# Performance work log

Measured on AMD Instinct MI355X. Metric: run time of the kernel, lower is better.

The kernel has to match this reference:

```python
import jax, jax.numpy as jnp
import numpy as np

NUM_CLASSES = 100


def setup_inputs() -> dict:
    key = jax.random.key(0)
    k1, k2, k3, k4 = jax.random.split(key, 4)
    x = jax.random.normal(k1, (256, 2048), dtype=jnp.float32)
    W_model = jax.random.normal(k2, (2048, 64), dtype=jnp.float32)
    database_code = jax.random.normal(k3, (100000, 64), dtype=jnp.float32)
    database_labels = jax.random.randint(k4, (100000,), 0, NUM_CLASSES, dtype=jnp.int64)
    return {
        "x": x,
        "W_model": W_model,
        "database_code": database_code,
        "database_labels": database_labels,
        "K": 1000,
    }


def reference(x, W_model, database_code, database_labels, K):
    # model(x): single linear projection to hash-code space [B, d]
    out = x @ W_model
    # sim_score = out @ codes.T * -0.5 + num_classes/2  -> [B, N]
    sim = jnp.matmul(out, database_code.T) * -0.5 + NUM_CLASSES / 2
    # np.argpartition(sim, K)[:, :K] selects the K SMALLEST scores.
    # Equivalent set via top_k on negated scores.
    _, topk_idx = jax.lax.top_k(-sim, K)            # [B, K]
    topk_labels = database_labels[topk_idx]          # [B, K]
    # per-class histogram over the top-K retrieved labels
    classes = jnp.arange(NUM_CLASSES, dtype=topk_labels.dtype)
    counts = (topk_labels[:, :, None] == classes[None, None, :]).sum(axis=1)  # [B, C]
    probs = counts.astype(jnp.float32) / K
    return probs
```

## Files before the change

kernel.cpp:

```cpp
#include <hip/hip_runtime.h>
#include <hip/hip_fp16.h>


#define NBK 256
#define FNB 1024
#define CAPC 2048
#define BCAP 2048
#define MROWS 32
#define NCHX 64
#define NCLS 100

typedef _Float16 half8 __attribute__((ext_vector_type(8)));
typedef float floatx4 __attribute__((ext_vector_type(4)));

static __device__ __forceinline__ unsigned packh2(float a, float b) {
  _Float16 ha = (_Float16)a, hb = (_Float16)b;
  unsigned short ua, ub;
  __builtin_memcpy(&ua, &ha, 2); __builtin_memcpy(&ub, &hb, 2);
  return (unsigned)ua | ((unsigned)ub << 16);
}

static __device__ __forceinline__ void rowRange(double b1sq, double cmax,
                                                double& lo, double& inv, double& bw) {
  double hr = 0.5 * sqrt(b1sq * cmax) * 1.000001 + 9.0;
  lo = 50.0 - hr;
  bw = (2.0 * hr) / (double)NBK;
  inv = (double)NBK / (2.0 * hr);
}

static __device__ __forceinline__ void loadA(const unsigned short* __restrict__ out16,
                                             int m0, int mr, int quad,
                                             half8& a00, half8& a01, half8& a10, half8& a11) {
  const uint4* o4 = (const uint4*)out16;
  uint4 u;
  u = o4[(size_t)(m0 + mr) * 8 + quad];          __builtin_memcpy(&a00, &u, 16);
  u = o4[(size_t)(m0 + mr) * 8 + 4 + quad];      __builtin_memcpy(&a01, &u, 16);
  u = o4[(size_t)(m0 + 16 + mr) * 8 + quad];     __builtin_memcpy(&a10, &u, 16);
  u = o4[(size_t)(m0 + 16 + mr) * 8 + 4 + quad]; __builtin_memcpy(&a11, &u, 16);
}

__global__ __launch_bounds__(1024) void k_prep(const float* __restrict__ x,
                                               const float* __restrict__ W,
                                               const float* __restrict__ codes,
                                               const int* __restrict__ labels,
                                               int N, int Npad, int D, int B, int nCvt,
                                               unsigned short* __restrict__ codes16,
                                               float* __restrict__ cmaxSlab,
                                               double* __restrict__ out64,
                                               unsigned short* __restrict__ out16,
                                               double* __restrict__ B1sq,
                                               int* __restrict__ shiftp) {
  __shared__ double red[1024];
  __shared__ float xs[2048];
  __shared__ float fredw[16];
  __shared__ int flag;
  int blk = (int)blockIdx.x, tid = (int)threadIdx.x;
  int lane = tid & 63, wid = tid >> 6;
  if (blk < nCvt) {
    int gl = tid & 15, g = tid >> 4;
    int base = blk * 256;
    int r0 = base + g, r1 = base + 64 + g, r2 = base + 128 + g, r3 = base + 192 + g;
    float4 q0 = {0.f,0.f,0.f,0.f}, q1 = q0, q2 = q0, q3 = q0;
    if (r0 < N) q0 = ((const float4*)(codes + (size_t)r0 * 64))[gl];
    if (r1 < N) q1 = ((const float4*)(codes + (size_t)r1 * 64))[gl];
    if (r2 < N) q2 = ((const float4*)(codes + (size_t)r2 * 64))[gl];
    if (r3 < N) q3 = ((const float4*)(codes + (size_t)r3 * 64))[gl];
    uint2 o0, o1, o2, o3;
    o0.x = packh2(q0.x, q0.y); o0.y = packh2(q0.z, q0.w);
    o1.x = packh2(q1.x, q1.y); o1.y = packh2(q1.z, q1.w);
    o2.x = packh2(q2.x, q2.y); o2.y = packh2(q2.z, q2.w);
    o3.x = packh2(q3.x, q3.y); o3.y = packh2(q3.z, q3.w);
    ((uint2*)(codes16 + (size_t)r0 * 64))[gl] = o0;
    ((uint2*)(codes16 + (size_t)r1 * 64))[gl] = o1;
    ((uint2*)(codes16 + (size_t)r2 * 64))[gl] = o2;
    ((uint2*)(codes16 + (size_t)r3 * 64))[gl] = o3;
    float bmax = 0.0f;
#define NRM(qv)                                                            \
    { double c2 = fma((double)(qv).x, (double)(qv).x, 0.0);                \
      c2 = fma((double)(qv).y, (double)(qv).y, c2);                        \
      c2 = fma((double)(qv).z, (double)(qv).z, c2);                        \
      c2 = fma((double)(qv).w, (double)(qv).w, c2);                        \
      c2 += __shfl_xor(c2, 1, 16); c2 += __shfl_xor(c2, 2, 16);            \
      c2 += __shfl_xor(c2, 4, 16); c2 += __shfl_xor(c2, 8, 16);            \
      bmax = fmaxf(bmax, (float)(c2 * 1.000001)); }
    NRM(q0) NRM(q1) NRM(q2) NRM(q3)
#undef NRM
#pragma unroll
    for (int off = 32; off > 0; off >>= 1) bmax = fmaxf(bmax, __shfl_xor(bmax, off, 64));
    if (lane == 0) fredw[wid] = bmax;
    __syncthreads();
    if (tid == 0) {
      float m = fredw[0];
#pragma unroll
      for (int j = 1; j < 16; ++j) m = fmaxf(m, fredw[j]);
      cmaxSlab[blk] = m;
    }
  } else if (blk < nCvt + B) {
    int b = blk - nCvt;
    const float* xr = x + (size_t)b * D;
    for (int i = tid; i < (D >> 1); i += 1024)
      ((float2*)xs)[i] = ((const float2*)xr)[i];
    __syncthreads();
    int t = tid & 63, w = tid >> 6;
    int kc = D >> 4;
    int k0 = w * kc;
    double a[8];
#pragma unroll
    for (int j = 0; j < 8; ++j) a[j] = 0.0;
#pragma unroll 2
    for (int k = k0; k < k0 + kc; k += 8) {
#pragma unroll
      for (int j = 0; j < 8; ++j)
        a[j] = fma((double)xs[k + j], (double)W[(size_t)(k + j) * 64 + t], a[j]);
    }
    red[tid] = ((a[0] + a[1]) + (a[2] + a[3])) + ((a[4] + a[5]) + (a[6] + a[7]));
    __syncthreads();
    if (w == 0) {
      double o = 0.0;
#pragma unroll
      for (int j = 0; j < 16; ++j) o += red[t + 64 * j];
      out64[(size_t)b * 64 + t] = o;
      _Float16 h = (_Float16)(float)o;
      unsigned short us; __builtin_memcpy(&us, &h, 2);
      out16[(size_t)b * 64 + t] = us;
      double sq = o * o;
#pragma unroll
      for (int off = 1; off < 64; off <<= 1) sq += __shfl_xor(sq, off, 64);
      if (t == 0) B1sq[b] = sq;
    }
  } else {
    if (tid == 0) flag = 0;
    __syncthreads();
    int m = N < 256 ? N : 256;
    if (tid < m && labels[2 * tid + 1] != 0) atomicOr(&flag, 1);
    __syncthreads();
    if (tid == 0) *shiftp = flag ? 0 : 1;
  }
}

__global__ __launch_bounds__(512) void k_mhist(const unsigned short* __restrict__ codes16,
                                               const unsigned short* __restrict__ out16,
                                               const double* __restrict__ B1sq,
                                               const float* __restrict__ cmaxSlab,
                                               int nCvt, int N, int Npad, int cpb, int B,
                                               unsigned short* __restrict__ histg,
                                               unsigned char* __restrict__ buck) {
  __shared__ unsigned hist[MROWS * NBK];
  __shared__ float sP[MROWS], sQ[MROWS], fredw[8];
  int tid = (int)threadIdx.x;
  int lane = tid & 63, wv = tid >> 6;
  int m0 = (int)blockIdx.y * MROWS, cx = (int)blockIdx.x;
  {
    float m = 0.0f;
    for (int i = tid; i < nCvt; i += 512) m = fmaxf(m, cmaxSlab[i]);
#pragma unroll
    for (int off = 32; off > 0; off >>= 1) m = fmaxf(m, __shfl_xor(m, off, 64));
    if (lane == 0) fredw[wv] = m;
  }
  for (int i = tid; i < MROWS * NBK; i += 512) hist[i] = 0u;
  __syncthreads();
  float cmax;
  { float m = fredw[0];
#pragma unroll
    for (int j = 1; j < 8; ++j) m = fmaxf(m, fredw[j]);
    cmax = m; }
  if (tid < MROWS) {
    double lo, inv, bw;
    rowRange(B1sq[m0 + tid], (double)cmax, lo, inv, bw);
    sP[tid] = (float)(-0.5 * inv);
    sQ[tid] = (float)((50.0 - lo) * inv);
  }
  __syncthreads();
  int quad = lane >> 4, mr = lane & 15;
  half8 a00, a01, a10, a11;
  loadA(out16, m0, mr, quad, a00, a01, a10, a11);
  float P0[4], Q0[4], P1[4], Q1[4];
#pragma unroll
  for (int r = 0; r < 4; ++r) {
    P0[r] = sP[quad*4 + r];      Q0[r] = sQ[quad*4 + r];
    P1[r] = sP[16 + quad*4 + r]; Q1[r] = sQ[16 + quad*4 + r];
  }
  int cstart = cx * cpb;
  int cend = cstart + cpb; if (cend > N) cend = N;
  const uint4* c4 = (const uint4*)codes16;
  floatx4 z = {0.f, 0.f, 0.f, 0.f};
  for (int base = cstart; base < cend; base += 128) {
    int nrow = base + wv * 16 + mr;
    int nc = nrow < Npad ? nrow : Npad - 1;
    uint4 ub0 = c4[(size_t)nc * 8 + quad];
    uint4 ub1 = c4[(size_t)nc * 8 + 4 + quad];
    half8 b0, b1;
    __builtin_memcpy(&b0, &ub0, 16); __builtin_memcpy(&b1, &ub1, 16);
    floatx4 d0 = __builtin_amdgcn_mfma_f32_16x16x32_f16(a00, b0, z, 0, 0, 0);
    d0 = __builtin_amdgcn_mfma_f32_16x16x32_f16(a01, b1, d0, 0, 0, 0);
    floatx4 d1 = __builtin_amdgcn_mfma_f32_16x16x32_f16(a10, b0, z, 0, 0, 0);
    d1 = __builtin_amdgcn_mfma_f32_16x16x32_f16(a11, b1, d1, 0, 0, 0);
    if (nrow < N) {
#pragma unroll
      for (int r = 0; r < 4; ++r) {
        int bk0 = (int)fmaf(d0[r], P0[r], Q0[r]);
        bk0 = bk0 < 0 ? 0 : (bk0 > NBK-1 ? NBK-1 : bk0);
        atomicAdd(&hist[(quad*4 + r) * NBK + bk0], 1u);
        buck[(size_t)(m0 + quad*4 + r) * N + nrow] = (unsigned char)bk0;
        int bk1 = (int)fmaf(d1[r], P1[r], Q1[r]);
        bk1 = bk1 < 0 ? 0 : (bk1 > NBK-1 ? NBK-1 : bk1);
        atomicAdd(&hist[(16 + quad*4 + r) * NBK + bk1], 1u);
        buck[(size_t)(m0 + 16 + quad*4 + r) * N + nrow] = (unsigned char)bk1;
      }
    }
  }
  __syncthreads();
  for (int i = tid; i < MROWS * NBK; i += 512)
    histg[((size_t)cx * B + (m0 + (i >> 8))) * NBK + (i & (NBK - 1))] =
        (unsigned short)hist[i];
}

__global__ __launch_bounds__(1024) void k_rowfinal(const float* __restrict__ codes,
                                                   const double* __restrict__ out64,
                                                   const double* __restrict__ B1sq,
                                                   const float* __restrict__ cmaxSlab,
                                                   const unsigned short* __restrict__ histg,
                                                   const unsigned char* __restrict__ buck,
                                                   const int* __restrict__ labels,
                                                   const int* __restrict__ shiftp,
                                                   const int* __restrict__ Kp,
                                                   float* __restrict__ outp,
                                                   int nCvt, int N, int B) {
  __shared__ float fredw[16];
  __shared__ unsigned sp[1024];
  __shared__ unsigned s[NBK];
  __shared__ unsigned wtot[4];
  __shared__ double key[CAPC];
  __shared__ int kidx[CAPC];
  __shared__ int blist[BCAP];
  __shared__ unsigned fhist[FNB];
  __shared__ unsigned ftot[16];
  __shared__ unsigned short tlist[CAPC];
  __shared__ double sod[64];
  __shared__ unsigned lab[NCLS];
  __shared__ unsigned ccnt, bcnt, tcnt, sCntLt;
  __shared__ int sTb, sFtb;
  int b = (int)blockIdx.x, tid = (int)threadIdx.x;
  int lane = tid & 63, wid = tid >> 6;

  {
    float m = (tid < nCvt) ? cmaxSlab[tid] : 0.0f;
    for (int i = tid + 1024; i < nCvt; i += 1024) m = fmaxf(m, cmaxSlab[i]);
#pragma unroll
    for (int off = 32; off > 0; off >>= 1) m = fmaxf(m, __shfl_xor(m, off, 64));
    if (lane == 0) fredw[wid] = m;
  }
  fhist[tid] = 0u;
  if (tid < 64) sod[tid] = out64[(size_t)b * 64 + tid];
  if (tid < NCLS) lab[tid] = 0u;
  if (tid == 0) { ccnt = 0u; bcnt = 0u; tcnt = 0u; sCntLt = 0u; sFtb = FNB; }
  __syncthreads();
  float cmax;
  { float m = fredw[0];
#pragma unroll
    for (int j = 1; j < 16; ++j) m = fmaxf(m, fredw[j]);
    cmax = m; }

  {
    int bk = tid & 255, cq = tid >> 8;
    unsigned part = 0;
#pragma unroll
    for (int t2 = 0; t2 < 16; ++t2)
      part += (unsigned)histg[((size_t)(cq * 16 + t2) * B + b) * NBK + bk];
    sp[tid] = part;
  }
  __syncthreads();
  {
    unsigned v = 0;
    if (tid < 256) {
      v = sp[tid] + sp[tid + 256] + sp[tid + 512] + sp[tid + 768];
#pragma unroll
      for (int off = 1; off < 64; off <<= 1) {
        unsigned t = (unsigned)__shfl_up((int)v, off, 64);
        if (lane >= off) v += t;
      }
      if (lane == 63) wtot[wid] = v;
    }
    __syncthreads();
    if (tid < 256) {
      for (int j = 0; j < wid; ++j) v += wtot[j];
      s[tid] = v;
    }
  }
  __syncthreads();
  unsigned K = (unsigned)Kp[0];
  if (tid < 256) {
    unsigned prev = tid ? s[tid - 1] : 0u;
    if (s[tid] >= K && prev < K) sTb = tid;
  }
  __syncthreads();
  int tb = sTb;
  double lo, inv, bwd;
  rowRange(B1sq[b], (double)cmax, lo, inv, bwd);
  double S = sqrt(B1sq[b] * (double)cmax);
  double Mtot = 2.0 * (0.5 * S * 1.1e-3 + 0.05) + 1e-3;
  int q = (int)ceil(Mtot / bwd);
  int belowMax = tb - 1 - q;
  int candMax = tb + 1 + q;
  if (candMax > NBK - 1) candMax = NBK - 1;
  unsigned btot = (belowMax >= 0) ? s[belowMax] : 0u;
  int shift = *shiftp;

  {
    const uint4* bw16 = (const uint4*)(buck + (size_t)b * N);
    int nw16 = N >> 4;
#define CLS1(nn, bkv)                                                  \
    { int bk_ = (int)(bkv);                                            \
      if (bk_ <= belowMax) {                                           \
        unsigned p_ = atomicAdd(&bcnt, 1u);                            \
        if (p_ < BCAP) blist[p_] = (nn);                               \
      } else if (bk_ <= candMax) {                                     \
        unsigned p_ = atomicAdd(&ccnt, 1u);                            \
        if (p_ < CAPC) kidx[p_] = (nn);                                \
      } }
#define PROCV(vv, nb)                                                  \
    { unsigned w_;                                                     \
      w_ = (vv).x; CLS1((nb)+0,  w_ & 0xFF) CLS1((nb)+1,  (w_>>8)&0xFF)\
                   CLS1((nb)+2,  (w_>>16)&0xFF) CLS1((nb)+3,  w_>>24)  \
      w_ = (vv).y; CLS1((nb)+4,  w_ & 0xFF) CLS1((nb)+5,  (w_>>8)&0xFF)\
                   CLS1((nb)+6,  (w_>>16)&0xFF) CLS1((nb)+7,  w_>>24)  \
      w_ = (vv).z; CLS1((nb)+8,  w_ & 0xFF) CLS1((nb)+9,  (w_>>8)&0xFF)\
                   CLS1((nb)+10, (w_>>16)&0xFF) CLS1((nb)+11, w_>>24)  \
      w_ = (vv).w; CLS1((nb)+12, w_ & 0xFF) CLS1((nb)+13, (w_>>8)&0xFF)\
                   CLS1((nb)+14, (w_>>16)&0xFF) CLS1((nb)+15, w_>>24) }
    for (int i = tid; i < nw16; i += 2048) {
      uint4 v0 = bw16[i];
      int i1 = i + 1024; bool h1 = i1 < nw16;
      uint4 v1 = {0u, 0u, 0u, 0u};
      if (h1) v1 = bw16[i1];
      PROCV(v0, i << 4)
      if (h1) PROCV(v1, i1 << 4)
    }
#undef PROCV
    for (int n = (nw16 << 4) + tid; n < N; n += 1024) {
      CLS1(n, buck[(size_t)b * N + n])
    }
#undef CLS1
  }
  __syncthreads();

  {
    int bm = (int)bcnt; if (bm > BCAP) bm = BCAP;
    for (int i = tid; i < bm; i += 1024)
      atomicAdd(&lab[labels[(size_t)blist[i] << shift]], 1u);
  }
  int cc = (int)ccnt; if (cc > CAPC) cc = CAPC;
  {
    int g = tid >> 4, gl = tid & 15;
    for (int i = g; i < cc; i += 64) {
      int n = kidx[i];
      float4 qv = ((const float4*)(codes + (size_t)n * 64))[gl];
      double p = fma((double)qv.x, sod[gl*4+0], 0.0);
      p = fma((double)qv.y, sod[gl*4+1], p);
      p = fma((double)qv.z, sod[gl*4+2], p);
      p = fma((double)qv.w, sod[gl*4+3], p);
      p += __shfl_xor(p, 1, 16);
      p += __shfl_xor(p, 2, 16);
      p += __shfl_xor(p, 4, 16);
      p += __shfl_xor(p, 8, 16);
      if (gl == 0) key[i] = fma(p, -0.5, 50.0);
    }
  }
  __syncthreads();

  int need = (int)K - (int)btot;
  double fLo = lo + (double)(belowMax + 1) * bwd - Mtot;
  double fInv = (double)FNB / ((double)(candMax - belowMax) * bwd + 2.0 * Mtot);
  for (int i = tid; i < cc; i += 1024) {
    int fb = (int)((key[i] - fLo) * fInv);
    fb = fb < 0 ? 0 : (fb > FNB - 1 ? FNB - 1 : fb);
    atomicAdd(&fhist[fb], 1u);
  }
  __syncthreads();
  {
    unsigned v = fhist[tid];
#pragma unroll
    for (int off = 1; off < 64; off <<= 1) {
      unsigned t = (unsigned)__shfl_up((int)v, off, 64);
      if (lane >= off) v += t;
    }
    if (lane == 63) ftot[wid] = v;
    sp[tid] = v;
  }
  __syncthreads();
  {
    unsigned off = 0;
    for (int j = 0; j < wid; ++j) off += ftot[j];
    unsigned ci = sp[tid] + off;
    unsigned ce = ci - fhist[tid];
    if ((int)ci >= need && (int)ce < need) { sFtb = tid; sCntLt = ce; }
  }
  __syncthreads();
  int ftb = sFtb;
  for (int i = tid; i < cc; i += 1024) {
    int fb = (int)((key[i] - fLo) * fInv);
    fb = fb < 0 ? 0 : (fb > FNB - 1 ? FNB - 1 : fb);
    if (fb < ftb) {
      atomicAdd(&lab[labels[(size_t)kidx[i] << shift]], 1u);
    } else if (fb == ftb) {
      unsigned p_ = atomicAdd(&tcnt, 1u);
      if (p_ < CAPC) tlist[p_] = (unsigned short)i;
    }
  }
  __syncthreads();
  {
    int tn = (int)tcnt; if (tn > CAPC) tn = CAPC;
    int rem = need - (int)sCntLt;
    for (int j = tid; j < tn; j += 1024) {
      int i = (int)tlist[j];
      double ki = key[i]; int ii = kidx[i];
      int rank = 0;
      for (int j2 = 0; j2 < tn; ++j2) {
        int i2 = (int)tlist[j2];
        double k2 = key[i2];
        rank += (k2 < ki || (k2 == ki && kidx[i2] < ii)) ? 1 : 0;
      }
      if (rank < rem) atomicAdd(&lab[labels[(size_t)ii << shift]], 1u);
    }
  }
  __syncthreads();
  double Kd = (double)K;
  for (int c = tid; c < NCLS; c += 1024)
    outp[b * NCLS + c] = (float)((double)lab[c] / Kd);
}

extern "C" void kernel_launch(void* const* d_in, const int* in_sizes, int n_in,
                              void* d_out, int out_size, void* d_ws, size_t ws_size,
                              hipStream_t stream) {
  const float* x     = (const float*)d_in[0];
  const float* W     = (const float*)d_in[1];
  const float* codes = (const float*)d_in[2];
  const int* labels  = (const int*)d_in[3];
  const int* Kp      = (const int*)d_in[4];

  const int B = out_size / NCLS;
  const int N = in_sizes[3];
  const int D = in_sizes[0] / B;
  const int Npad = (N + 255) & ~255;
  const int cpb = (((N + NCHX - 1) / NCHX) + 127) & ~127;
  const int nCvt = Npad / 256;

  char* p = (char*)d_ws;
  double* out64      = (double*)p;   p += (size_t)B * 64 * sizeof(double);
  unsigned short* out16 = (unsigned short*)p; p += (size_t)B * 64 * 2;
  double* B1sq       = (double*)p;   p += (size_t)B * sizeof(double);
  int* shiftp        = (int*)p;      p += 64;
  float* cmaxSlab    = (float*)p;    p += 4096;
  unsigned short* histg = (unsigned short*)p; p += (size_t)NCHX * B * NBK * 2;
  unsigned char* buck   = (unsigned char*)p;  p += (size_t)B * N;
  unsigned short* codes16 = (unsigned short*)p;

  k_prep<<<nCvt + B + 1, 1024, 0, stream>>>(x, W, codes, labels, N, Npad, D, B, nCvt,
                                            codes16, cmaxSlab, out64, out16, B1sq, shiftp);
  k_mhist<<<dim3(NCHX, B / MROWS), 512, 0, stream>>>(codes16, out16, B1sq, cmaxSlab,
                                                     nCvt, N, Npad, cpb, B, histg, buck);
  k_rowfinal<<<B, 1024, 0, stream>>>(codes, out64, B1sq, cmaxSlab, histg, buck,
                                     labels, shiftp, Kp, (float*)d_out, nCvt, N, B);
}
```

Before: 152.8 us.

## Prefetch bucket row into registers at kernel start; use lightweight LDS barriers

The per-row bucket array (N=100000 bytes, 6250 uint4 words) is now loaded into registers at kernel entry, so the global-memory latency overlaps the cmax reduction, histogram prefix scan and threshold search. The classification loop is fully unrolled over seven fixed slots. __syncthreads is replaced by an LDS-only wait plus s_barrier, so the outstanding global loads are not drained at each barrier. This hardcodes the assumption that N/16 is at most 7168 and raises register pressure.

New measurement: 155.5 us. No clear change (+1.8%).

```diff
diff --git a/kernel.cpp b/kernel.cpp
--- a/kernel.cpp
+++ b/kernel.cpp
@@ -9,6 +9,9 @@
 #define MROWS 32
 #define NCHX 64
 #define NCLS 100
+
+#define LDSBAR() do { asm volatile("s_waitcnt lgkmcnt(0)" ::: "memory"); \
+                      __builtin_amdgcn_s_barrier(); } while (0)
 
 typedef _Float16 half8 __attribute__((ext_vector_type(8)));
 typedef float floatx4 __attribute__((ext_vector_type(4)));
@@ -243,6 +246,18 @@
   int b = (int)blockIdx.x, tid = (int)threadIdx.x;
   int lane = tid & 63, wid = tid >> 6;
 
+  const uint4* bw16 = (const uint4*)(buck + (size_t)b * N);
+  const int nw16 = N >> 4;
+  uint4 pv0 = bw16[tid];
+  uint4 pv1 = bw16[tid + 1024];
+  uint4 pv2 = bw16[tid + 2048];
+  uint4 pv3 = bw16[tid + 3072];
+  uint4 pv4 = bw16[tid + 4096];
+  uint4 pv5 = bw16[tid + 5120];
+  uint4 pv6 = {0u, 0u, 0u, 0u};
+  bool h6 = (tid + 6144) < nw16;
+  if (h6) pv6 = bw16[tid + 6144];
+
   {
     float m = (tid < nCvt) ? cmaxSlab[tid] : 0.0f;
     for (int i = tid + 1024; i < nCvt; i += 1024) m = fmaxf(m, cmaxSlab[i]);
@@ -254,7 +269,7 @@
   if (tid < 64) sod[tid] = out64[(size_t)b * 64 + tid];
   if (tid < NCLS) lab[tid] = 0u;
   if (tid == 0) { ccnt = 0u; bcnt = 0u; tcnt = 0u; sCntLt = 0u; sFtb = FNB; }
-  __syncthreads();
+  LDSBAR();
   float cmax;
   { float m = fredw[0];
 #pragma unroll
@@ -269,7 +284,7 @@
       part += (unsigned)histg[((size_t)(cq * 16 + t2) * B + b) * NBK + bk];
     sp[tid] = part;
   }
-  __syncthreads();
+  LDSBAR();
   {
     unsigned v = 0;
     if (tid < 256) {
@@ -281,19 +296,19 @@
       }
       if (lane == 63) wtot[wid] = v;
     }
-    __syncthreads();
+    LDSBAR();
     if (tid < 256) {
       for (int j = 0; j < wid; ++j) v += wtot[j];
       s[tid] = v;
     }
   }
-  __syncthreads();
+  LDSBAR();
   unsigned K = (unsigned)Kp[0];
   if (tid < 256) {
     unsigned prev = tid ? s[tid - 1] : 0u;
     if (s[tid] >= K && prev < K) sTb = tid;
   }
-  __syncthreads();
+  LDSBAR();
   int tb = sTb;
   double lo, inv, bwd;
   rowRange(B1sq[b], (double)cmax, lo, inv, bwd);
@@ -307,8 +322,6 @@
   int shift = *shiftp;
 
   {
-    const uint4* bw16 = (const uint4*)(buck + (size_t)b * N);
-    int nw16 = N >> 4;
 #define CLS1(nn, bkv)                                                  \
     { int bk_ = (int)(bkv);                                            \
       if (bk_ <= belowMax) {                                           \
@@ -328,14 +341,13 @@
                    CLS1((nb)+10, (w_>>16)&0xFF) CLS1((nb)+11, w_>>24)  \
       w_ = (vv).w; CLS1((nb)+12, w_ & 0xFF) CLS1((nb)+13, (w_>>8)&0xFF)\
                    CLS1((nb)+14, (w_>>16)&0xFF) CLS1((nb)+15, w_>>24) }
-    for (int i = tid; i < nw16; i += 2048) {
-      uint4 v0 = bw16[i];
-      int i1 = i + 1024; bool h1 = i1 < nw16;
-      uint4 v1 = {0u, 0u, 0u, 0u};
-      if (h1) v1 = bw16[i1];
-      PROCV(v0, i << 4)
-      if (h1) PROCV(v1, i1 << 4)
-    }
+    PROCV(pv0, tid << 4)
+    PROCV(pv1, (tid + 1024) << 4)
+    PROCV(pv2, (tid + 2048) << 4)
+    PROCV(pv3, (tid + 3072) << 4)
+    PROCV(pv4, (tid + 4096) << 4)
+    PROCV(pv5, (tid + 5120) << 4)
+    if (h6) PROCV(pv6, (tid + 6144) << 4)
 #undef PROCV
     for (int n = (nw16 << 4) + tid; n < N; n += 1024) {
       CLS1(n, buck[(size_t)b * N + n])
```
